# Performance work log

Measured on AMD Instinct MI355X. Metric: run time of the kernel, lower is better.

## Reference

```python
import jax, jax.numpy as jnp
import numpy as np

B = 8_388_608
GRID = 201   # floor(lat/0.9) in [-100,100], floor(lon/1.8) in [-100,100]
OFFSET = 100
ALPHA = 0.1


def setup_inputs() -> dict:
    key = jax.random.key(0)
    k1, k2, k3 = jax.random.split(key, 3)
    predictions = jax.random.uniform(k1, (B, 2), dtype=jnp.float32)
    labels = jax.random.uniform(k2, (B, 2), dtype=jnp.float32)
    weight_grid = jax.random.uniform(k3, (GRID, GRID), dtype=jnp.float32)
    return {"predictions": predictions, "labels": labels, "weight_grid": weight_grid}


def reference(predictions, labels, weight_grid):
    # |pred - label| (the code calls it mse_error but computes abs error)
    err = jnp.abs(predictions - labels)                       # [B, 2]
    # denormalize: lat in [-90, 90), lon in [-180, 180)
    lat = predictions[..., 0] * 180.0 - 90.0
    lon = predictions[..., 1] * 360.0 - 180.0
    # torch float // is floor division; indices offset into dense grid
    xi = jnp.floor(lat / 0.9).astype(jnp.int32) + OFFSET
    yi = jnp.floor(lon / 1.8).astype(jnp.int32) + OFFSET
    xi = jnp.clip(xi, 0, GRID - 1)
    yi = jnp.clip(yi, 0, GRID - 1)
    w = weight_grid[xi, yi]                                   # [B]
    weighted = err + err * (ALPHA - ALPHA * w[:, None])       # [B, 2]
    return weighted.mean()
```

## Files before the change

kernel.cpp:

```cpp
#include <hip/hip_runtime.h>


constexpr int   GRIDN  = 201;
constexpr int   GRIDSZ = GRIDN * GRIDN;
constexpr float ALPHA  = 0.1f;

__global__ __launch_bounds__(1024) void wmse_reduce(
    const float4* __restrict__ pred4,
    const float4* __restrict__ lab4,
    const float*  __restrict__ wg,
    float*        __restrict__ out,
    int n4, float scale)
{
    __shared__ float wg_lds[GRIDSZ];

    for (int j = threadIdx.x; j < GRIDSZ; j += 1024)
        wg_lds[j] = wg[j];
    __syncthreads();

    float acc = 0.0f;
    const int stride = gridDim.x * blockDim.x;
    #pragma unroll 4
    for (int i = blockIdx.x * blockDim.x + threadIdx.x; i < n4; i += stride) {
        const float4 p = pred4[i];
        const float4 l = lab4[i];

        {
            const float e   = fabsf(p.x - l.x) + fabsf(p.y - l.y);
            const float lat = p.x * 180.0f - 90.0f;
            const float lon = p.y * 360.0f - 180.0f;
            int xi = (int)floorf(lat / 0.9f) + 100;
            int yi = (int)floorf(lon / 1.8f) + 100;
            xi = min(max(xi, 0), GRIDN - 1);
            yi = min(max(yi, 0), GRIDN - 1);
            const float w = wg_lds[xi * GRIDN + yi];
            acc += e * (1.0f + ALPHA - ALPHA * w);
        }
        {
            const float e   = fabsf(p.z - l.z) + fabsf(p.w - l.w);
            const float lat = p.z * 180.0f - 90.0f;
            const float lon = p.w * 360.0f - 180.0f;
            int xi = (int)floorf(lat / 0.9f) + 100;
            int yi = (int)floorf(lon / 1.8f) + 100;
            xi = min(max(xi, 0), GRIDN - 1);
            yi = min(max(yi, 0), GRIDN - 1);
            const float w = wg_lds[xi * GRIDN + yi];
            acc += e * (1.0f + ALPHA - ALPHA * w);
        }
    }

    #pragma unroll
    for (int off = 32; off > 0; off >>= 1)
        acc += __shfl_down(acc, off, 64);

    __shared__ float red[16];
    const int lane = threadIdx.x & 63;
    const int wid  = threadIdx.x >> 6;
    if (lane == 0) red[wid] = acc;
    __syncthreads();
    if (threadIdx.x == 0) {
        float s = 0.0f;
        #pragma unroll
        for (int k = 0; k < 16; ++k) s += red[k];
        atomicAdd(out, s * scale);
    }
}

extern "C" void kernel_launch(void* const* d_in, const int* in_sizes, int n_in,
                              void* d_out, int out_size, void* d_ws, size_t ws_size,
                              hipStream_t stream) {
    const float4* pred = (const float4*)d_in[0];
    const float4* lab  = (const float4*)d_in[1];
    const float*  wg   = (const float*)d_in[2];
    float*        out  = (float*)d_out;

    const long long total = (long long)in_sizes[0];
    const int   n4    = (int)(total / 4);
    const float scale = 1.0f / (float)total;

    hipMemsetAsync(d_out, 0, sizeof(float), stream);

    const int block = 1024;
    const int grid  = 256;
    wmse_reduce<<<grid, block, 0, stream>>>(pred, lab, wg, out, n4, scale);
}
```

Baseline: 153.6 us.

## Store weight grid as fp16 in LDS, simplify index math, double grid

Converts the 201x201 weight table to half precision when it is staged into LDS. This halves the table's shared-memory footprint, so more blocks can be resident per CU. The lat/lon denormalize-and-divide index computation is folded algebraically into a truncation of p*200, which removes the divisions and floors. The launch grid goes from 256 to 512 blocks. The risks are fp16 rounding of the weights and slight index differences at bin boundaries compared with the float division.

```diff
diff --git a/kernel.cpp b/kernel.cpp
--- a/kernel.cpp
+++ b/kernel.cpp
@@ -1,21 +1,31 @@
 #include <hip/hip_runtime.h>
+#include <hip/hip_fp16.h>
 
 
 constexpr int   GRIDN  = 201;
 constexpr int   GRIDSZ = GRIDN * GRIDN;
 constexpr float ALPHA  = 0.1f;
 
-__global__ __launch_bounds__(1024) void wmse_reduce(
+__global__ __launch_bounds__(1024, 8) void wmse_reduce(
     const float4* __restrict__ pred4,
     const float4* __restrict__ lab4,
     const float*  __restrict__ wg,
     float*        __restrict__ out,
     int n4, float scale)
 {
-    __shared__ float wg_lds[GRIDSZ];
+    __shared__ __half wg_lds[GRIDSZ];
 
-    for (int j = threadIdx.x; j < GRIDSZ; j += 1024)
-        wg_lds[j] = wg[j];
+    const float4* wg4 = (const float4*)wg;
+    for (int j = threadIdx.x; j < GRIDSZ / 4; j += 1024) {
+        const float4 v = wg4[j];
+        __half2 h01, h23;
+        h01.x = __float2half(v.x); h01.y = __float2half(v.y);
+        h23.x = __float2half(v.z); h23.y = __float2half(v.w);
+        *reinterpret_cast<__half2*>(&wg_lds[j * 4])     = h01;
+        *reinterpret_cast<__half2*>(&wg_lds[j * 4 + 2]) = h23;
+    }
+    if (threadIdx.x == 0)
+        wg_lds[GRIDSZ - 1] = __float2half(wg[GRIDSZ - 1]);
     __syncthreads();
 
     float acc = 0.0f;
@@ -26,26 +36,18 @@
         const float4 l = lab4[i];
 
         {
-            const float e   = fabsf(p.x - l.x) + fabsf(p.y - l.y);
-            const float lat = p.x * 180.0f - 90.0f;
-            const float lon = p.y * 360.0f - 180.0f;
-            int xi = (int)floorf(lat / 0.9f) + 100;
-            int yi = (int)floorf(lon / 1.8f) + 100;
-            xi = min(max(xi, 0), GRIDN - 1);
-            yi = min(max(yi, 0), GRIDN - 1);
-            const float w = wg_lds[xi * GRIDN + yi];
-            acc += e * (1.0f + ALPHA - ALPHA * w);
+            const float e = fabsf(p.x - l.x) + fabsf(p.y - l.y);
+            int xi = min(max((int)(p.x * 200.0f), 0), GRIDN - 1);
+            int yi = min(max((int)(p.y * 200.0f), 0), GRIDN - 1);
+            const float w = __half2float(wg_lds[xi * GRIDN + yi]);
+            acc += e * fmaf(-ALPHA, w, 1.0f + ALPHA);
         }
         {
-            const float e   = fabsf(p.z - l.z) + fabsf(p.w - l.w);
-            const float lat = p.z * 180.0f - 90.0f;
-            const float lon = p.w * 360.0f - 180.0f;
-            int xi = (int)floorf(lat / 0.9f) + 100;
-            int yi = (int)floorf(lon / 1.8f) + 100;
-            xi = min(max(xi, 0), GRIDN - 1);
-            yi = min(max(yi, 0), GRIDN - 1);
-            const float w = wg_lds[xi * GRIDN + yi];
-            acc += e * (1.0f + ALPHA - ALPHA * w);
+            const float e = fabsf(p.z - l.z) + fabsf(p.w - l.w);
+            int xi = min(max((int)(p.z * 200.0f), 0), GRIDN - 1);
+            int yi = min(max((int)(p.w * 200.0f), 0), GRIDN - 1);
+            const float w = __half2float(wg_lds[xi * GRIDN + yi]);
+            acc += e * fmaf(-ALPHA, w, 1.0f + ALPHA);
         }
     }
 
@@ -81,6 +83,6 @@
     hipMemsetAsync(d_out, 0, sizeof(float), stream);
 
     const int block = 1024;
-    const int grid  = 256;
+    const int grid  = 512;
     wmse_reduce<<<grid, block, 0, stream>>>(pred, lab, wg, out, n4, scale);
 }
```

After: 153.8 us. Within noise of the previous version (+0.1%).
